# Performance work log

Hardware: AMD Instinct MI355X
Metric: run time of the kernel (lower is better)

## Reference

```python
import jax, jax.numpy as jnp
import numpy as np

B, H, W, C = 8, 256, 256, 64
M1, M2 = 32, 32
SCALE = 1.0 / (C * C)


def setup_inputs() -> dict:
    key = jax.random.key(0)
    ku, k1, k2, k3, k4 = jax.random.split(key, 5)
    u = jax.random.normal(ku, (B, H, W, C), dtype=jnp.float32)
    wshape = (C, C, M1, M2)
    w_pos_r = SCALE * jax.random.normal(k1, wshape, dtype=jnp.float32)
    w_pos_i = SCALE * jax.random.normal(k2, wshape, dtype=jnp.float32)
    w_neg_r = SCALE * jax.random.normal(k3, wshape, dtype=jnp.float32)
    w_neg_i = SCALE * jax.random.normal(k4, wshape, dtype=jnp.float32)
    return {"u": u, "w_pos_r": w_pos_r, "w_pos_i": w_pos_i,
            "w_neg_r": w_neg_r, "w_neg_i": w_neg_i}


def _compl_mul2d(inp, weights):
    # inp: [B, m1, m2, Cin] complex; weights: [Cin, Cout, m1, m2] complex
    return jnp.einsum('bxyi,ioxy->bxyo', inp, weights)


def reference(u, w_pos_r, w_pos_i, w_neg_r, w_neg_i):
    b, h, w, c = u.shape
    wf = w // 2 + 1  # rfft size along W
    u_ft = jnp.fft.rfft2(u, axes=(1, 2))  # [B, H, Wf, C] complex
    w_pos = jax.lax.complex(w_pos_r, w_pos_i)
    w_neg = jax.lax.complex(w_neg_r, w_neg_i)
    top = _compl_mul2d(u_ft[:, :M1, :M2, :], w_pos)   # low positive freqs
    bot = _compl_mul2d(u_ft[:, h - M1:, :M2, :], w_neg)  # low negative freqs
    # out_ft zero-initialized, only truncated modes populated.
    # (Original allocates [B,H,W,C] but irfft2 with s=(H,W) only reads
    #  the first W//2+1 columns, which equals this [B,H,Wf,C] tensor.)
    out_ft = jnp.zeros((b, h, wf, c), dtype=u_ft.dtype)
    out_ft = out_ft.at[:, :M1, :M2, :].set(top)
    out_ft = out_ft.at[:, h - M1:, :M2, :].set(bot)
    # out_ft[:, -M1:M1] assignment in original is an empty slice (M1 <= H/2): no-op.
    return jnp.fft.irfft2(out_ft, s=(h, w), axes=(1, 2)).astype(u.dtype)
```

## Files before the change

### kernel.cpp

```cpp
#include <hip/hip_runtime.h>
#include <math.h>

#define BB 8
#define HH 256
#define WW 256
#define CC 64

__device__ inline void cmac(float2& a, float tx, float ty, float2 v) {
    a.x += tx * v.x - ty * v.y;
    a.y += tx * v.y + ty * v.x;
}
__device__ inline void fma4(float4& a, float s, float4 v) {
    a.x += s * v.x; a.y += s * v.y; a.z += s * v.z; a.w += s * v.w;
}

__global__ __launch_bounds__(256) void k_tw(float2* __restrict__ Tf,
                                            float2* __restrict__ Ti,
                                            float* __restrict__ Ty,
                                            float* __restrict__ T2) {
    int e = blockIdx.x * 256 + threadIdx.x;
    if (e < 16384) {
        int x = e >> 6;
        int j = e & 63;
        int kxa = j + ((j >> 5) * 192);
        int tt = (kxa * x) & 255;
        float ang = (float)tt * (6.283185307179586f / 256.0f);
        float s, c;
        sincosf(ang, &s, &c);
        Tf[(size_t)x * 64 + j] = make_float2(c, -s);
        const float k = 2.0f / 65536.0f;
        Ti[(size_t)j * 256 + x] = make_float2(c * k, s * k);
    } else {
        int f = e - 16384;
        if (f < 8192) {
            int yp = f >> 6;
            int col = f & 63;
            int par = (col >> 5) & 1;
            int cs = (col >> 4) & 1;
            int m = col & 15;
            int ky = 2 * m + par;
            int tt = (ky * yp) & 255;
            float ang = (float)tt * (6.283185307179586f / 256.0f);
            float s, c;
            sincosf(ang, &s, &c);
            Ty[f] = cs ? -s : c;
        } else {
            int g = f - 8192;
            int pi = g >> 12;
            int j = (g >> 7) & 31;
            int p = g & 127;
            int m = j >> 1, ri = j & 1;
            int ky = 2 * m + pi;
            int tt = (ky * p) & 255;
            float ang = (float)tt * (6.283185307179586f / 256.0f);
            float s, c;
            sincosf(ang, &s, &c);
            T2[g] = ri ? -s : c;
        }
    }
}

__global__ __launch_bounds__(256, 2) void k_fwd_y(const float* __restrict__ u,
                                                  const float* __restrict__ Ty,
                                                  float2* __restrict__ V) {
    __shared__ float ue[2][4][8 * 68];
    __shared__ float uo[2][4][8 * 68];
    __shared__ float Tt[2][8 * 68];

    int t = threadIdx.x;
    int bx = blockIdx.x;
    int b = bx >> 6;
    int x4 = (bx & 63) * 4;
    int r = t >> 6;
    int l = t & 63;
    int x = x4 + r;
    int i8 = (l & 7) * 8;
    int w = l >> 3;
    int p = w & 1;
    int kq = w >> 1;
    int yy = l >> 3;
    int c0 = (l & 7) * 8;
    int trow = t >> 5;
    int tc = (t & 31) * 2;

    const float* ub = u + ((size_t)(b * HH + x)) * (WW * CC);

    float4 aR[4], aI[4], bR[4], bI[4];
    #pragma unroll
    for (int m = 0; m < 4; ++m) {
        aR[m] = make_float4(0,0,0,0); aI[m] = make_float4(0,0,0,0);
        bR[m] = make_float4(0,0,0,0); bI[m] = make_float4(0,0,0,0);
    }

    float4 L0, L1, H0, H1;
    float2 TV;

    {
        const float* plo = ub + (size_t)yy * CC + c0;
        const float* phi = plo + 128 * CC;
        L0 = *(const float4*)(plo);
        L1 = *(const float4*)(plo + 4);
        H0 = *(const float4*)(phi);
        H1 = *(const float4*)(phi + 4);
        TV = *(const float2*)(Ty + (size_t)trow * 64 + tc);
        int wb = yy * 68 + c0;
        float* uer = ue[0][r];
        float* uor = uo[0][r];
        *(float4*)(uer + wb)     = make_float4(L0.x+H0.x, L0.y+H0.y, L0.z+H0.z, L0.w+H0.w);
        *(float4*)(uer + wb + 4) = make_float4(L1.x+H1.x, L1.y+H1.y, L1.z+H1.z, L1.w+H1.w);
        *(float4*)(uor + wb)     = make_float4(L0.x-H0.x, L0.y-H0.y, L0.z-H0.z, L0.w-H0.w);
        *(float4*)(uor + wb + 4) = make_float4(L1.x-H1.x, L1.y-H1.y, L1.z-H1.z, L1.w-H1.w);
        *(float2*)(&Tt[0][trow * 68 + tc]) = TV;
    }
    __syncthreads();

    for (int yt = 0; yt < 16; ++yt) {
        int cur = yt & 1;
        if (yt < 15) {
            const float* plo = ub + (size_t)((yt + 1) * 8 + yy) * CC + c0;
            const float* phi = plo + 128 * CC;
            L0 = *(const float4*)(plo);
            L1 = *(const float4*)(plo + 4);
            H0 = *(const float4*)(phi);
            H1 = *(const float4*)(phi + 4);
            TV = *(const float2*)(Ty + (size_t)((yt + 1) * 8 + trow) * 64 + tc);
        }

        const float* uplane = p ? uo[cur][r] : ue[cur][r];
        const float* ttab = Tt[cur];
        #pragma unroll
        for (int y2 = 0; y2 < 8; ++y2) {
            const float* tb = ttab + y2 * 68 + p * 32 + kq * 2;
            float2 c01 = *(const float2*)(tb);
            float2 c89 = *(const float2*)(tb + 8);
            float2 s01 = *(const float2*)(tb + 16);
            float2 s89 = *(const float2*)(tb + 24);
            const float* up = uplane + y2 * 68 + i8;
            float4 u0 = *(const float4*)(up);
            float4 u1 = *(const float4*)(up + 4);
            fma4(aR[0], c01.x, u0);  fma4(bR[0], c01.x, u1);
            fma4(aI[0], s01.x, u0);  fma4(bI[0], s01.x, u1);
            fma4(aR[1], c01.y, u0);  fma4(bR[1], c01.y, u1);
            fma4(aI[1], s01.y, u0);  fma4(bI[1], s01.y, u1);
            fma4(aR[2], c89.x, u0);  fma4(bR[2], c89.x, u1);
            fma4(aI[2], s89.x, u0);  fma4(bI[2], s89.x, u1);
            fma4(aR[3], c89.y, u0);  fma4(bR[3], c89.y, u1);
            fma4(aI[3], s89.y, u0);  fma4(bI[3], s89.y, u1);
        }

        if (yt < 15) {
            int nb = cur ^ 1;
            int wb = yy * 68 + c0;
            float* uer = ue[nb][r];
            float* uor = uo[nb][r];
            *(float4*)(uer + wb)     = make_float4(L0.x+H0.x, L0.y+H0.y, L0.z+H0.z, L0.w+H0.w);
            *(float4*)(uer + wb + 4) = make_float4(L1.x+H1.x, L1.y+H1.y, L1.z+H1.z, L1.w+H1.w);
            *(float4*)(uor + wb)     = make_float4(L0.x-H0.x, L0.y-H0.y, L0.z-H0.z, L0.w-H0.w);
            *(float4*)(uor + wb + 4) = make_float4(L1.x-H1.x, L1.y-H1.y, L1.z-H1.z, L1.w-H1.w);
            *(float2*)(&Tt[nb][trow * 68 + tc]) = TV;
        }
        __syncthreads();
    }

    int mv[4] = {2 * kq, 2 * kq + 1, 2 * kq + 8, 2 * kq + 9};
    #pragma unroll
    for (int mi = 0; mi < 4; ++mi) {
        int ky = 2 * mv[mi] + p;
        float2* vp = V + (size_t)(b * HH + x) * 2048 + ky * 64 + i8;
        *(float4*)(vp)     = make_float4(aR[mi].x, aI[mi].x, aR[mi].y, aI[mi].y);
        *(float4*)(vp + 2) = make_float4(aR[mi].z, aI[mi].z, aR[mi].w, aI[mi].w);
        *(float4*)(vp + 4) = make_float4(bR[mi].x, bI[mi].x, bR[mi].y, bI[mi].y);
        *(float4*)(vp + 6) = make_float4(bR[mi].z, bI[mi].z, bR[mi].w, bI[mi].w);
    }
}

__global__ __launch_bounds__(256) void k_fwd_x(const float2* __restrict__ Tf,
                                               const float2* __restrict__ V,
                                               float2* __restrict__ U) {
    __shared__ float sRe[2 * 2048];
    __shared__ float sIm[2 * 2048];
    __shared__ float2 Ts[32 * 16];

    int bx = blockIdx.x;
    int jq = bx >> 8;
    int ky = bx & 31;
    int b  = (bx >> 5) & 7;
    int t = threadIdx.x;
    int jr = t >> 5;
    int ir = t & 31;

    float2 a00 = {0,0}, a01 = {0,0}, a10 = {0,0}, a11 = {0,0};

    const float2* vb = V + (size_t)b * (HH * 2048) + ky * 64;
    int vrow = t >> 3;
    int vcol = (t & 7) * 8;
    int tjj = (t & 7) * 2;
    int parOff = (jr & 1) * 2048;

    for (int x0 = 0; x0 < 128; x0 += 32) {
        const float2* plo = vb + (size_t)(x0 + vrow) * 2048 + vcol;
        const float2* phi = plo + 128 * 2048;
        float4 l0 = *(const float4*)(plo);
        float4 l1 = *(const float4*)(plo + 2);
        float4 l2 = *(const float4*)(plo + 4);
        float4 l3 = *(const float4*)(plo + 6);
        float4 h0 = *(const float4*)(phi);
        float4 h1 = *(const float4*)(phi + 2);
        float4 h2 = *(const float4*)(phi + 4);
        float4 h3 = *(const float4*)(phi + 6);
        float4 tv = *(const float4*)(Tf + (size_t)(x0 + vrow) * 64 + jq * 16 + tjj);

        __syncthreads();
        *(float4*)&Ts[vrow * 16 + tjj] = tv;
        int wb = vrow * 64 + vcol;
        *(float4*)(sRe + wb)            = make_float4(l0.x+h0.x, l0.z+h0.z, l1.x+h1.x, l1.z+h1.z);
        *(float4*)(sRe + wb + 4)        = make_float4(l2.x+h2.x, l2.z+h2.z, l3.x+h3.x, l3.z+h3.z);
        *(float4*)(sIm + wb)            = make_float4(l0.y+h0.y, l0.w+h0.w, l1.y+h1.y, l1.w+h1.w);
        *(float4*)(sIm + wb + 4)        = make_float4(l2.y+h2.y, l2.w+h2.w, l3.y+h3.y, l3.w+h3.w);
        *(float4*)(sRe + 2048 + wb)     = make_float4(l0.x-h0.x, l0.z-h0.z, l1.x-h1.x, l1.z-h1.z);
        *(float4*)(sRe + 2048 + wb + 4) = make_float4(l2.x-h2.x, l2.z-h2.z, l3.x-h3.x, l3.z-h3.z);
        *(float4*)(sIm + 2048 + wb)     = make_float4(l0.y-h0.y, l0.w-h0.w, l1.y-h1.y, l1.w-h1.w);
        *(float4*)(sIm + 2048 + wb + 4) = make_float4(l2.y-h2.y, l2.w-h2.w, l3.y-h3.y, l3.w-h3.w);
        __syncthreads();

        #pragma unroll
        for (int xx = 0; xx < 32; ++xx) {
            float2 t0 = Ts[xx * 16 + jr];
            float2 t1 = Ts[xx * 16 + jr + 8];
            const float* re = sRe + parOff + xx * 64;
            const float* im = sIm + parOff + xx * 64;
            float vr0 = re[ir], vr1 = re[ir + 32];
            float vi0 = im[ir], vi1 = im[ir + 32];
            a00.x += t0.x*vr0 - t0.y*vi0;  a00.y += t0.x*vi0 + t0.y*vr0;
            a01.x += t0.x*vr1 - t0.y*vi1;  a01.y += t0.x*vi1 + t0.y*vr1;
            a10.x += t1.x*vr0 - t1.y*vi0;  a10.y += t1.x*vi0 + t1.y*vr0;
            a11.x += t1.x*vr1 - t1.y*vi1;  a11.y += t1.x*vi1 + t1.y*vr1;
        }
    }

    int j0 = jq * 16 + jr;
    float2* u0 = U + ((size_t)(j0 * 32 + ky) * 8 + b) * 64 + ir;
    u0[0]  = a00;
    u0[32] = a01;
    float2* u1 = U + ((size_t)((j0 + 8) * 32 + ky) * 8 + b) * 64 + ir;
    u1[0]  = a10;
    u1[32] = a11;
}

__global__ __launch_bounds__(256) void k_modew(const float* __restrict__ wpr,
                                               const float* __restrict__ wpi,
                                               const float* __restrict__ wnr,
                                               const float* __restrict__ wni,
                                               const float2* __restrict__ U,
                                               float2* __restrict__ OF) {
    __shared__ float2 uS[4 * 8 * 64];
    __shared__ float2 wS[2][4 * 8 * 32];

    int bx = blockIdx.x;
    int j   = bx & 63;
    int kyt = (bx >> 6) & 7;
    int oh  = bx >> 9;
    int ky0 = kyt * 4;
    int sel = j >> 5, kxl = j & 31;
    const float* sr = sel ? wnr : wpr;
    const float* si = sel ? wni : wpi;
    int tid = threadIdx.x;

    int o32 = tid & 31;
    int bh  = tid >> 5;
    int irS = tid >> 5;
    int ooS = tid & 31;

    {
        const float4* up4 = (const float4*)(U + (size_t)(j * 32 + ky0) * 512);
        float4* uS4 = (float4*)uS;
        #pragma unroll
        for (int k = 0; k < 4; ++k) uS4[tid + 256 * k] = up4[tid + 256 * k];
    }
    float4 r0, q0;
    {
        size_t base = (((size_t)(irS * 64 + oh * 32 + ooS)) * 32 + kxl) * 32 + ky0;
        r0 = *(const float4*)(sr + base);
        q0 = *(const float4*)(si + base);
        float2* wrow = wS[0] + irS * 32 + ooS;
        wrow[0 * 256] = make_float2(r0.x, q0.x);
        wrow[1 * 256] = make_float2(r0.y, q0.y);
        wrow[2 * 256] = make_float2(r0.z, q0.z);
        wrow[3 * 256] = make_float2(r0.w, q0.w);
    }
    __syncthreads();

    float2 acc[4];
    #pragma unroll
    for (int k = 0; k < 4; ++k) acc[k] = make_float2(0.f, 0.f);

    for (int it = 0; it < 8; ++it) {
        int cur = it & 1;
        if (it < 7) {
            int ig = (it + 1) * 8 + irS;
            size_t base = (((size_t)(ig * 64 + oh * 32 + ooS)) * 32 + kxl) * 32 + ky0;
            r0 = *(const float4*)(sr + base);
            q0 = *(const float4*)(si + base);
        }

        const float2* wcur = wS[cur];
        #pragma unroll
        for (int ir = 0; ir < 8; ++ir) {
            int ig = it * 8 + ir;
            #pragma unroll
            for (int ky = 0; ky < 4; ++ky) {
                float2 wv = wcur[ky * 256 + ir * 32 + o32];
                float2 uv = uS[ky * 512 + bh * 64 + ig];
                acc[ky].x += uv.x * wv.x - uv.y * wv.y;
                acc[ky].y += uv.x * wv.y + uv.y * wv.x;
            }
        }

        if (it < 7) {
            float2* wrow = wS[cur ^ 1] + irS * 32 + ooS;
            wrow[0 * 256] = make_float2(r0.x, q0.x);
            wrow[1 * 256] = make_float2(r0.y, q0.y);
            wrow[2 * 256] = make_float2(r0.z, q0.z);
            wrow[3 * 256] = make_float2(r0.w, q0.w);
        }
        __syncthreads();
    }

    int og = oh * 32 + o32;
    #pragma unroll
    for (int ky = 0; ky < 4; ++ky) {
        OF[((size_t)(bh * 32 + ky0 + ky) * 64 + j) * 64 + og] = acc[ky];
    }
}

__global__ __launch_bounds__(256) void k_inv_x(const float2* __restrict__ Ti,
                                               const float2* __restrict__ OF,
                                               float2* __restrict__ A) {
    __shared__ float2 Ts[32 * 32];
    __shared__ float2 Os[32 * 64];

    int bx = blockIdx.x;
    int xt = bx >> 8;
    int ky = bx & 31;
    int b  = (bx >> 5) & 7;
    int t = threadIdx.x;
    int or_ = t & 15;
    int xr = t >> 4;

    float2 acc[2][2][4];
    #pragma unroll
    for (int pa = 0; pa < 2; ++pa)
        #pragma unroll
        for (int p = 0; p < 2; ++p)
            #pragma unroll
            for (int q = 0; q < 4; ++q) acc[pa][p][q] = make_float2(0.f, 0.f);

    const float2* ofb = OF + (size_t)(b * 32 + ky) * 4096;
    int sj = t >> 3;
    int sx = (t & 7) * 4;
    int so = (t & 7) * 8;

    for (int kh = 0; kh < 2; ++kh) {
        const float2* tsrc = Ti + (size_t)(kh * 32 + sj) * 256 + xt * 32 + sx;
        float4 t0 = *(const float4*)(tsrc);
        float4 t1 = *(const float4*)(tsrc + 2);
        const float2* osrc = ofb + (size_t)(kh * 32 + sj) * 64 + so;
        float4 o0 = *(const float4*)(osrc);
        float4 o1 = *(const float4*)(osrc + 2);
        float4 o2 = *(const float4*)(osrc + 4);
        float4 o3 = *(const float4*)(osrc + 6);

        __syncthreads();
        *(float4*)&Ts[sj * 32 + sx]     = t0;
        *(float4*)&Ts[sj * 32 + sx + 2] = t1;
        float2* od = &Os[sj * 64 + so];
        *(float4*)(od)     = o0;
        *(float4*)(od + 2) = o1;
        *(float4*)(od + 4) = o2;
        *(float4*)(od + 6) = o3;
        __syncthreads();

        #pragma unroll
        for (int jj = 0; jj < 32; ++jj) {
            float4 tp = *(const float4*)&Ts[jj * 32 + xr * 2];
            float2 q0 = Os[jj * 64 + or_];
            float2 q1 = Os[jj * 64 + or_ + 16];
            float2 q2 = Os[jj * 64 + or_ + 32];
            float2 q3 = Os[jj * 64 + or_ + 48];
            const int pa = jj & 1;
            cmac(acc[pa][0][0], tp.x, tp.y, q0);
            cmac(acc[pa][0][1], tp.x, tp.y, q1);
            cmac(acc[pa][0][2], tp.x, tp.y, q2);
            cmac(acc[pa][0][3], tp.x, tp.y, q3);
            cmac(acc[pa][1][0], tp.z, tp.w, q0);
            cmac(acc[pa][1][1], tp.z, tp.w, q1);
            cmac(acc[pa][1][2], tp.z, tp.w, q2);
            cmac(acc[pa][1][3], tp.z, tp.w, q3);
        }
    }

    float sc = (ky == 0) ? 0.5f : 1.0f;
    #pragma unroll
    for (int p = 0; p < 2; ++p) {
        int x = xt * 32 + xr * 2 + p;
        float2* alo = A + ((size_t)(b * 256 + x) * 32 + ky) * 64 + or_;
        float2* ahi = A + ((size_t)(b * 256 + x + 128) * 32 + ky) * 64 + or_;
        #pragma unroll
        for (int q = 0; q < 4; ++q) {
            float2 se = acc[0][p][q], so2 = acc[1][p][q];
            alo[16 * q] = make_float2((se.x + so2.x) * sc, (se.y + so2.y) * sc);
            ahi[16 * q] = make_float2((se.x - so2.x) * sc, (se.y - so2.y) * sc);
        }
    }
}

__global__ __launch_bounds__(256) void k_inv_y(const float* __restrict__ T2g,
                                               const float2* __restrict__ A,
                                               float* __restrict__ out) {
    __shared__ float As[64 * 68];
    __shared__ float T2s[64 * 132];

    int t = threadIdx.x;
    int b = blockIdx.x >> 8;
    int x = blockIdx.x & 255;

    {
        int ky = t >> 3;
        int oc = (t & 7) * 8;
        const float2* ap = A + (size_t)(b * 256 + x) * 2048 + ky * 64 + oc;
        float4 g0 = *(const float4*)(ap);
        float4 g1 = *(const float4*)(ap + 2);
        float4 g2 = *(const float4*)(ap + 4);
        float4 g3 = *(const float4*)(ap + 6);
        int pi = ky & 1, m = ky >> 1;
        float* re = As + ((pi * 32) + 2 * m) * 68 + oc;
        float* im = As + ((pi * 32) + 2 * m + 1) * 68 + oc;
        *(float4*)(re)     = make_float4(g0.x, g0.z, g1.x, g1.z);
        *(float4*)(re + 4) = make_float4(g2.x, g2.z, g3.x, g3.z);
        *(float4*)(im)     = make_float4(g0.y, g0.w, g1.y, g1.w);
        *(float4*)(im + 4) = make_float4(g2.y, g2.w, g3.y, g3.w);
    }
    {
        int row = t >> 2;
        int c = (t & 3) * 32;
        const float* tg = T2g + (size_t)row * 128 + c;
        float* td = T2s + row * 132 + c;
        #pragma unroll
        for (int k = 0; k < 8; ++k) {
            float4 q = *(const float4*)(tg + 4 * k);
            *(float4*)(td + 4 * k) = q;
        }
    }
    __syncthreads();

    int pr = t >> 4;
    int o4 = (t & 15) * 4;

    float4 acc[2][8];
    #pragma unroll
    for (int pi = 0; pi < 2; ++pi)
        #pragma unroll
        for (int pp = 0; pp < 8; ++pp) acc[pi][pp] = make_float4(0,0,0,0);

    #pragma unroll
    for (int pi = 0; pi < 2; ++pi) {
        #pragma unroll
        for (int jj = 0; jj < 32; ++jj) {
            const float* trow = T2s + (pi * 32 + jj) * 132 + pr * 8;
            float4 ta = *(const float4*)(trow);
            float4 tb = *(const float4*)(trow + 4);
            float4 av = *(const float4*)(As + (pi * 32 + jj) * 68 + o4);
            fma4(acc[pi][0], ta.x, av);
            fma4(acc[pi][1], ta.y, av);
            fma4(acc[pi][2], ta.z, av);
            fma4(acc[pi][3], ta.w, av);
            fma4(acc[pi][4], tb.x, av);
            fma4(acc[pi][5], tb.y, av);
            fma4(acc[pi][6], tb.z, av);
            fma4(acc[pi][7], tb.w, av);
        }
    }

    float* op = out + (size_t)(b * 256 + x) * (256 * 64);
    #pragma unroll
    for (int pp = 0; pp < 8; ++pp) {
        int p = pr * 8 + pp;
        float4 e = acc[0][pp], d = acc[1][pp];
        *(float4*)(op + (size_t)p * 64 + o4)
            = make_float4(e.x+d.x, e.y+d.y, e.z+d.z, e.w+d.w);
        *(float4*)(op + (size_t)(p + 128) * 64 + o4)
            = make_float4(e.x-d.x, e.y-d.y, e.z-d.z, e.w-d.w);
    }
}

extern "C" void kernel_launch(void* const* d_in, const int* in_sizes, int n_in,
                              void* d_out, int out_size, void* d_ws, size_t ws_size,
                              hipStream_t stream) {
    const float* u   = (const float*)d_in[0];
    const float* wpr = (const float*)d_in[1];
    const float* wpi = (const float*)d_in[2];
    const float* wnr = (const float*)d_in[3];
    const float* wni = (const float*)d_in[4];
    float* out = (float*)d_out;

    char* ws = (char*)d_ws;
    float2* U  = (float2*)(ws);
    float2* OF = (float2*)(ws + 8388608);
    float2* V  = (float2*)(ws + 16777216);
    float2* A  = V;
    float2* Tf = (float2*)(ws + 50331648);
    float2* Ti = (float2*)(ws + 50331648 + 131072);
    float*  Ty = (float*)(ws + 50331648 + 262144);
    float*  T2 = (float*)(ws + 50331648 + 262144 + 32768);

    k_tw<<<128, 256, 0, stream>>>(Tf, Ti, Ty, T2);
    k_fwd_y<<<512, 256, 0, stream>>>(u, Ty, V);
    k_fwd_x<<<1024, 256, 0, stream>>>(Tf, V, U);
    k_modew<<<1024, 256, 0, stream>>>(wpr, wpi, wnr, wni, U, OF);
    k_inv_x<<<1024, 256, 0, stream>>>(Ti, OF, A);
    k_inv_y<<<BB * HH, 256, 0, stream>>>(T2, A, out);
}
```

Before: 215.4 us.

## Double-buffer shared-memory tiles in forward and inverse x-DFT kernels

Both k_fwd_x and k_inv_x now use halved tile depths with two shared-memory buffers. Global loads for the next tile are issued before computing on the current tile and written to the other buffer afterward, leaving one barrier per iteration. The goal is to hide global-load latency behind the complex multiply-accumulate loop. The cost is more iterations with shorter inner loops and some extra registers held across the compute phase.

```diff
diff --git a/kernel.cpp b/kernel.cpp
--- a/kernel.cpp
+++ b/kernel.cpp
@@ -177,9 +177,9 @@
 __global__ __launch_bounds__(256) void k_fwd_x(const float2* __restrict__ Tf,
                                                const float2* __restrict__ V,
                                                float2* __restrict__ U) {
-    __shared__ float sRe[2 * 2048];
-    __shared__ float sIm[2 * 2048];
-    __shared__ float2 Ts[32 * 16];
+    __shared__ float sRe[2][2 * 1024];
+    __shared__ float sIm[2][2 * 1024];
+    __shared__ float2 Ts[2][16 * 16];
 
     int bx = blockIdx.x;
     int jq = bx >> 8;
@@ -192,43 +192,52 @@
     float2 a00 = {0,0}, a01 = {0,0}, a10 = {0,0}, a11 = {0,0};
 
     const float2* vb = V + (size_t)b * (HH * 2048) + ky * 64;
-    int vrow = t >> 3;
-    int vcol = (t & 7) * 8;
-    int tjj = (t & 7) * 2;
-    int parOff = (jr & 1) * 2048;
-
-    for (int x0 = 0; x0 < 128; x0 += 32) {
-        const float2* plo = vb + (size_t)(x0 + vrow) * 2048 + vcol;
+    int vrow = t >> 4;
+    int vcol = (t & 15) * 4;
+    int tjj  = t & 15;
+    int parOff = (jr & 1) * 1024;
+
+    float4 l0, l1, h0, h1;
+    float2 tv;
+
+    {
+        const float2* plo = vb + (size_t)vrow * 2048 + vcol;
         const float2* phi = plo + 128 * 2048;
-        float4 l0 = *(const float4*)(plo);
-        float4 l1 = *(const float4*)(plo + 2);
-        float4 l2 = *(const float4*)(plo + 4);
-        float4 l3 = *(const float4*)(plo + 6);
-        float4 h0 = *(const float4*)(phi);
-        float4 h1 = *(const float4*)(phi + 2);
-        float4 h2 = *(const float4*)(phi + 4);
-        float4 h3 = *(const float4*)(phi + 6);
-        float4 tv = *(const float4*)(Tf + (size_t)(x0 + vrow) * 64 + jq * 16 + tjj);
-
-        __syncthreads();
-        *(float4*)&Ts[vrow * 16 + tjj] = tv;
+        l0 = *(const float4*)(plo);
+        l1 = *(const float4*)(plo + 2);
+        h0 = *(const float4*)(phi);
+        h1 = *(const float4*)(phi + 2);
+        tv = *(const float2*)((const float*)(Tf + (size_t)vrow * 64 + jq * 16 + tjj));
         int wb = vrow * 64 + vcol;
-        *(float4*)(sRe + wb)            = make_float4(l0.x+h0.x, l0.z+h0.z, l1.x+h1.x, l1.z+h1.z);
-        *(float4*)(sRe + wb + 4)        = make_float4(l2.x+h2.x, l2.z+h2.z, l3.x+h3.x, l3.z+h3.z);
-        *(float4*)(sIm + wb)            = make_float4(l0.y+h0.y, l0.w+h0.w, l1.y+h1.y, l1.w+h1.w);
-        *(float4*)(sIm + wb + 4)        = make_float4(l2.y+h2.y, l2.w+h2.w, l3.y+h3.y, l3.w+h3.w);
-        *(float4*)(sRe + 2048 + wb)     = make_float4(l0.x-h0.x, l0.z-h0.z, l1.x-h1.x, l1.z-h1.z);
-        *(float4*)(sRe + 2048 + wb + 4) = make_float4(l2.x-h2.x, l2.z-h2.z, l3.x-h3.x, l3.z-h3.z);
-        *(float4*)(sIm + 2048 + wb)     = make_float4(l0.y-h0.y, l0.w-h0.w, l1.y-h1.y, l1.w-h1.w);
-        *(float4*)(sIm + 2048 + wb + 4) = make_float4(l2.y-h2.y, l2.w-h2.w, l3.y-h3.y, l3.w-h3.w);
-        __syncthreads();
-
-        #pragma unroll
-        for (int xx = 0; xx < 32; ++xx) {
-            float2 t0 = Ts[xx * 16 + jr];
-            float2 t1 = Ts[xx * 16 + jr + 8];
-            const float* re = sRe + parOff + xx * 64;
-            const float* im = sIm + parOff + xx * 64;
+        *(float4*)(&sRe[0][wb])        = make_float4(l0.x+h0.x, l0.z+h0.z, l1.x+h1.x, l1.z+h1.z);
+        *(float4*)(&sIm[0][wb])        = make_float4(l0.y+h0.y, l0.w+h0.w, l1.y+h1.y, l1.w+h1.w);
+        *(float4*)(&sRe[0][1024 + wb]) = make_float4(l0.x-h0.x, l0.z-h0.z, l1.x-h1.x, l1.z-h1.z);
+        *(float4*)(&sIm[0][1024 + wb]) = make_float4(l0.y-h0.y, l0.w-h0.w, l1.y-h1.y, l1.w-h1.w);
+        Ts[0][vrow * 16 + tjj] = tv;
+    }
+    __syncthreads();
+
+    for (int xt = 0; xt < 8; ++xt) {
+        int cur = xt & 1;
+        if (xt < 7) {
+            const float2* plo = vb + (size_t)((xt + 1) * 16 + vrow) * 2048 + vcol;
+            const float2* phi = plo + 128 * 2048;
+            l0 = *(const float4*)(plo);
+            l1 = *(const float4*)(plo + 2);
+            h0 = *(const float4*)(phi);
+            h1 = *(const float4*)(phi + 2);
+            tv = *(const float2*)((const float*)(Tf + (size_t)((xt + 1) * 16 + vrow) * 64 + jq * 16 + tjj));
+        }
+
+        const float2* tss = Ts[cur];
+        const float* reb = &sRe[cur][parOff];
+        const float* imb = &sIm[cur][parOff];
+        #pragma unroll
+        for (int xx = 0; xx < 16; ++xx) {
+            float2 t0 = tss[xx * 16 + jr];
+            float2 t1 = tss[xx * 16 + jr + 8];
+            const float* re = reb + xx * 64;
+            const float* im = imb + xx * 64;
             float vr0 = re[ir], vr1 = re[ir + 32];
             float vi0 = im[ir], vi1 = im[ir + 32];
             a00.x += t0.x*vr0 - t0.y*vi0;  a00.y += t0.x*vi0 + t0.y*vr0;
@@ -236,6 +245,17 @@
             a10.x += t1.x*vr0 - t1.y*vi0;  a10.y += t1.x*vi0 + t1.y*vr0;
             a11.x += t1.x*vr1 - t1.y*vi1;  a11.y += t1.x*vi1 + t1.y*vr1;
         }
+
+        if (xt < 7) {
+            int nb = cur ^ 1;
+            int wb = vrow * 64 + vcol;
+            *(float4*)(&sRe[nb][wb])        = make_float4(l0.x+h0.x, l0.z+h0.z, l1.x+h1.x, l1.z+h1.z);
+            *(float4*)(&sIm[nb][wb])        = make_float4(l0.y+h0.y, l0.w+h0.w, l1.y+h1.y, l1.w+h1.w);
+            *(float4*)(&sRe[nb][1024 + wb]) = make_float4(l0.x-h0.x, l0.z-h0.z, l1.x-h1.x, l1.z-h1.z);
+            *(float4*)(&sIm[nb][1024 + wb]) = make_float4(l0.y-h0.y, l0.w-h0.w, l1.y-h1.y, l1.w-h1.w);
+            Ts[nb][vrow * 16 + tjj] = tv;
+        }
+        __syncthreads();
     }
 
     int j0 = jq * 16 + jr;
@@ -336,8 +356,8 @@
 __global__ __launch_bounds__(256) void k_inv_x(const float2* __restrict__ Ti,
                                                const float2* __restrict__ OF,
                                                float2* __restrict__ A) {
-    __shared__ float2 Ts[32 * 32];
-    __shared__ float2 Os[32 * 64];
+    __shared__ float2 Ts[2][16 * 32];
+    __shared__ float2 Os[2][16 * 64];
 
     int bx = blockIdx.x;
     int xt = bx >> 8;
@@ -356,37 +376,42 @@
             for (int q = 0; q < 4; ++q) acc[pa][p][q] = make_float2(0.f, 0.f);
 
     const float2* ofb = OF + (size_t)(b * 32 + ky) * 4096;
-    int sj = t >> 3;
-    int sx = (t & 7) * 4;
-    int so = (t & 7) * 8;
-
-    for (int kh = 0; kh < 2; ++kh) {
-        const float2* tsrc = Ti + (size_t)(kh * 32 + sj) * 256 + xt * 32 + sx;
-        float4 t0 = *(const float4*)(tsrc);
-        float4 t1 = *(const float4*)(tsrc + 2);
-        const float2* osrc = ofb + (size_t)(kh * 32 + sj) * 64 + so;
-        float4 o0 = *(const float4*)(osrc);
-        float4 o1 = *(const float4*)(osrc + 2);
-        float4 o2 = *(const float4*)(osrc + 4);
-        float4 o3 = *(const float4*)(osrc + 6);
-
-        __syncthreads();
-        *(float4*)&Ts[sj * 32 + sx]     = t0;
-        *(float4*)&Ts[sj * 32 + sx + 2] = t1;
-        float2* od = &Os[sj * 64 + so];
+    int sj = t >> 4;
+    int sx = (t & 15) * 2;
+    int so = (t & 15) * 4;
+
+    float4 t0, o0, o1;
+
+    {
+        t0 = *(const float4*)(Ti + (size_t)sj * 256 + xt * 32 + sx);
+        const float2* osrc = ofb + (size_t)sj * 64 + so;
+        o0 = *(const float4*)(osrc);
+        o1 = *(const float4*)(osrc + 2);
+        *(float4*)&Ts[0][sj * 32 + sx] = t0;
+        float2* od = &Os[0][sj * 64 + so];
         *(float4*)(od)     = o0;
         *(float4*)(od + 2) = o1;
-        *(float4*)(od + 4) = o2;
-        *(float4*)(od + 6) = o3;
-        __syncthreads();
-
-        #pragma unroll
-        for (int jj = 0; jj < 32; ++jj) {
-            float4 tp = *(const float4*)&Ts[jj * 32 + xr * 2];
-            float2 q0 = Os[jj * 64 + or_];
-            float2 q1 = Os[jj * 64 + or_ + 16];
-            float2 q2 = Os[jj * 64 + or_ + 32];
-            float2 q3 = Os[jj * 64 + or_ + 48];
+    }
+    __syncthreads();
+
+    for (int kt = 0; kt < 4; ++kt) {
+        int cur = kt & 1;
+        if (kt < 3) {
+            t0 = *(const float4*)(Ti + (size_t)((kt + 1) * 16 + sj) * 256 + xt * 32 + sx);
+            const float2* osrc = ofb + (size_t)((kt + 1) * 16 + sj) * 64 + so;
+            o0 = *(const float4*)(osrc);
+            o1 = *(const float4*)(osrc + 2);
+        }
+
+        const float2* tsb = Ts[cur];
+        const float2* osb = Os[cur];
+        #pragma unroll
+        for (int jj = 0; jj < 16; ++jj) {
+            float4 tp = *(const float4*)&tsb[jj * 32 + xr * 2];
+            float2 q0 = osb[jj * 64 + or_];
+            float2 q1 = osb[jj * 64 + or_ + 16];
+            float2 q2 = osb[jj * 64 + or_ + 32];
+            float2 q3 = osb[jj * 64 + or_ + 48];
             const int pa = jj & 1;
             cmac(acc[pa][0][0], tp.x, tp.y, q0);
             cmac(acc[pa][0][1], tp.x, tp.y, q1);
@@ -397,6 +422,15 @@
             cmac(acc[pa][1][2], tp.z, tp.w, q2);
             cmac(acc[pa][1][3], tp.z, tp.w, q3);
         }
+
+        if (kt < 3) {
+            int nb = cur ^ 1;
+            *(float4*)&Ts[nb][sj * 32 + sx] = t0;
+            float2* od = &Os[nb][sj * 64 + so];
+            *(float4*)(od)     = o0;
+            *(float4*)(od + 2) = o1;
+        }
+        __syncthreads();
     }
 
     float sc = (ky == 0) ? 0.5f : 1.0f;
```

Result: slower. 230.0 us (+6.8%).
